# Optimization experiments

Hardware: AMD Instinct MI355X
Metric: run time of the kernel (lower is better)

The kernel has to match this reference:

```python
import jax, jax.numpy as jnp
import numpy as np

LN_EPS = 1e-5
ROPE_BASE = 10000.0


def rotate_half(x):
    # x: [..., d]; split into two halves (matches einops '(j d)->j d', j=2)
    d2 = x.shape[-1] // 2
    x1, x2 = x[..., :d2], x[..., d2:]
    return jnp.concatenate((-x2, x1), axis=-1)


def rotary_pos_emb(n, head_dim, dtype=jnp.float32):
    inv_freq = 1.0 / (ROPE_BASE ** (jnp.arange(0, head_dim, 2, dtype=jnp.float32) / head_dim))
    t = jnp.arange(n, dtype=jnp.float32)
    freqs = jnp.einsum('i,j->ij', t, inv_freq)          # [n, d/2]
    return jnp.concatenate((freqs, freqs), axis=-1).astype(dtype)  # [n, d]


def apply_rotary(pos, t):
    return t * jnp.cos(pos) + rotate_half(t) * jnp.sin(pos)


def setup_inputs() -> dict:
    key = jax.random.key(0)
    ks = jax.random.split(key, 4)
    b, n, dm = 2, 4096, 2048
    x = jax.random.normal(ks[0], (b, n, dm), dtype=jnp.float32)
    wq = jax.random.normal(ks[1], (dm, dm), dtype=jnp.float32) * (dm ** -0.5)
    wk = jax.random.normal(ks[2], (dm, dm), dtype=jnp.float32) * (dm ** -0.5)
    wv = jax.random.normal(ks[3], (dm, dm), dtype=jnp.float32) * (dm ** -0.5)
    return {
        'x': x,
        'ln_gamma': jnp.ones((dm,), jnp.float32),
        'ln_beta': jnp.zeros((dm,), jnp.float32),
        'wq': wq, 'wk': wk, 'wv': wv,
        'num_heads': 16,
    }


def reference(x, ln_gamma, ln_beta, wq, wk, wv, num_heads):
    b, n, dm = x.shape
    hd = dm // num_heads
    # LayerNorm (eps=1e-5, torch default)
    mu = jnp.mean(x, axis=-1, keepdims=True)
    var = jnp.mean(jnp.square(x - mu), axis=-1, keepdims=True)
    xn = (x - mu) * jax.lax.rsqrt(var + LN_EPS) * ln_gamma + ln_beta
    # QKV projections (nn.Linear, bias=False => x @ W.T; weights stored as [out,in])
    q = jnp.einsum('bnd,ed->bne', xn, wq)
    k = jnp.einsum('bnd,ed->bne', xn, wk)
    v = jnp.einsum('bnd,ed->bne', xn, wv)
    # b n (h d) -> b h n d
    split = lambda t: t.reshape(b, n, num_heads, hd).transpose(0, 2, 1, 3)
    q, k, v = split(q), split(k), split(v)
    pos = rotary_pos_emb(n, hd, x.dtype)  # [n, hd], broadcasts over b,h
    q = apply_rotary(pos, q)
    k = apply_rotary(pos, k)
    return q, k, v
```

## Files before the change

kernel.cpp:

```cpp
#include <hip/hip_runtime.h>
#include <hip/hip_bf16.h>


typedef float f32x4 __attribute__((ext_vector_type(4)));
typedef __bf16 bf16x8 __attribute__((ext_vector_type(8)));
typedef __bf16 bf16x4 __attribute__((ext_vector_type(4)));

#define DM    2048
#define NSEQ  4096
#define NH    16
#define HD    128
#define NROWS 8192
#define MAT_ELEMS (2ull*NH*NSEQ*HD)

typedef __attribute__((address_space(1))) const void GV;
typedef __attribute__((address_space(3))) void LV;
__device__ __forceinline__ void gload_lds16(const void* g, void* l) {
    __builtin_amdgcn_global_load_lds((GV*)g, (LV*)l, 16, 0, 0);
}

__global__ __launch_bounds__(256)
void lncvt_kernel(const float* __restrict__ x, const float* __restrict__ g,
                  const float* __restrict__ be,
                  const float* __restrict__ wq, const float* __restrict__ wk,
                  const float* __restrict__ wv,
                  __bf16* __restrict__ xnb, __bf16* __restrict__ wb) {
    int bid = blockIdx.x;
    int tid = threadIdx.x;
    if (bid < NROWS) {
        int row = bid;
        const float4* xr = (const float4*)(x + (size_t)row * DM);
        float4 v0 = xr[tid];
        float4 v1 = xr[tid + 256];
        float s  = v0.x + v0.y + v0.z + v0.w + v1.x + v1.y + v1.z + v1.w;
        float ss = v0.x*v0.x + v0.y*v0.y + v0.z*v0.z + v0.w*v0.w
                 + v1.x*v1.x + v1.y*v1.y + v1.z*v1.z + v1.w*v1.w;
#pragma unroll
        for (int o = 32; o > 0; o >>= 1) {
            s  += __shfl_down(s, o);
            ss += __shfl_down(ss, o);
        }
        __shared__ float red[10];
        int wave = tid >> 6, lane = tid & 63;
        if (lane == 0) { red[wave] = s; red[4 + wave] = ss; }
        __syncthreads();
        if (tid == 0) {
            float S  = red[0] + red[1] + red[2] + red[3];
            float SS = red[4] + red[5] + red[6] + red[7];
            float mu  = S * (1.0f / DM);
            float var = SS * (1.0f / DM) - mu * mu;
            red[8] = mu;
            red[9] = rsqrtf(var + 1e-5f);
        }
        __syncthreads();
        float mu = red[8], rs = red[9];

        const float4* gp = (const float4*)g;
        const float4* bp = (const float4*)be;
        bf16x4* orow = (bf16x4*)(xnb + (size_t)row * DM);
        {
            float4 g0 = gp[tid], b0 = bp[tid];
            bf16x4 o;
            o[0] = (__bf16)((v0.x - mu) * rs * g0.x + b0.x);
            o[1] = (__bf16)((v0.y - mu) * rs * g0.y + b0.y);
            o[2] = (__bf16)((v0.z - mu) * rs * g0.z + b0.z);
            o[3] = (__bf16)((v0.w - mu) * rs * g0.w + b0.w);
            orow[tid] = o;
        }
        {
            float4 g1 = gp[tid + 256], b1 = bp[tid + 256];
            bf16x4 o;
            o[0] = (__bf16)((v1.x - mu) * rs * g1.x + b1.x);
            o[1] = (__bf16)((v1.y - mu) * rs * g1.y + b1.y);
            o[2] = (__bf16)((v1.z - mu) * rs * g1.z + b1.z);
            o[3] = (__bf16)((v1.w - mu) * rs * g1.w + b1.w);
            orow[tid + 256] = o;
        }
    } else {
        int cb = bid - NROWS;
        const float* a = (cb < 2048) ? wq : (cb < 4096) ? wk : wv;
        size_t base = ((size_t)(cb & 2047) * 256 + tid) * 8;
        float4 v0 = *(const float4*)(a + base);
        float4 v1 = *(const float4*)(a + base + 4);
        bf16x8 r;
        r[0] = (__bf16)v0.x; r[1] = (__bf16)v0.y; r[2] = (__bf16)v0.z; r[3] = (__bf16)v0.w;
        r[4] = (__bf16)v1.x; r[5] = (__bf16)v1.y; r[6] = (__bf16)v1.z; r[7] = (__bf16)v1.w;
        *(bf16x8*)(wb + (size_t)(cb >> 11) * 4194304 + base) = r;
    }
}


__device__ __forceinline__ void loadA4(bf16x8 (&a)[4][2], const __bf16* Sp,
                                       int base, int mb, int o0) {
#pragma unroll
    for (int mi = 0; mi < 4; mi++)
#pragma unroll
        for (int ks = 0; ks < 2; ks++)
            a[mi][ks] = *(const bf16x8*)(Sp + base + (mb + mi) * 1024 + (o0 ^ (ks * 32)));
}
__device__ __forceinline__ void loadB2(bf16x8 (&b)[2][2], const __bf16* Sp,
                                       int base, int cb, int o0) {
#pragma unroll
    for (int f = 0; f < 2; f++)
#pragma unroll
        for (int ks = 0; ks < 2; ks++)
            b[f][ks] = *(const bf16x8*)(Sp + base + (f * 16 + (cb >> 1) * 64) * 64 + (o0 ^ (ks * 32)));
}

template<int RB, int CB>
__device__ __forceinline__ void cluster(f32x4 (&acc)[8][4], bf16x8 (&a)[4][2],
                                        bf16x8 (&b)[2][2]) {
    __builtin_amdgcn_s_setprio(1);
#pragma unroll
    for (int mi = 0; mi < 4; mi++)
#pragma unroll
        for (int ni = 0; ni < 2; ni++)
#pragma unroll
            for (int ks = 0; ks < 2; ks++)
                acc[RB + mi][CB + ni] = __builtin_amdgcn_mfma_f32_16x16x32_bf16(
                    a[mi][ks], b[ni][ks], acc[RB + mi][CB + ni], 0, 0, 0);
    __builtin_amdgcn_s_setprio(0);
}

#define FENCE asm volatile("" ::: "memory")
#define BAR   do { FENCE; __builtin_amdgcn_s_barrier(); FENCE; } while (0)
#define VM8   asm volatile("s_waitcnt vmcnt(8)" ::: "memory")
#define VM0   asm volatile("s_waitcnt vmcnt(0)" ::: "memory")

#define STGA(P, kt, HF) do { \
    gload_lds16(pA + (size_t)((HF) * 64 + w * 8) * DM + (kt) * 64,       &As[P][((HF) * 8 + w) * 512]); \
    gload_lds16(pA + (size_t)((HF) * 64 + 128 + w * 8) * DM + (kt) * 64, &As[P][((HF) * 8 + 16 + w) * 512]); \
} while (0)
#define STGB(P, kt, HF) do { \
    gload_lds16(pB + (size_t)((HF) * 64 + w * 8) * DM + (kt) * 64,       &Bs[P][((HF) * 8 + w) * 512]); \
    gload_lds16(pB + (size_t)((HF) * 64 + 128 + w * 8) * DM + (kt) * 64, &Bs[P][((HF) * 8 + 16 + w) * 512]); \
} while (0)

#define KTILE(kt, P, SG, W) do { \
    W; BAR; \
    loadA4(a,  &As[P][0], baseA, 0, o0); \
    loadB2(b0, &Bs[P][0], baseB, 0, o0); \
    loadB2(b1, &Bs[P][0], baseB, 2, o0); \
    cluster<0, 0>(acc, a, b0); \
    cluster<0, 2>(acc, a, b1); \
    loadA4(a, &As[P][0], baseA, 4, o0); \
    cluster<4, 0>(acc, a, b0); \
    cluster<4, 2>(acc, a, b1); \
    BAR; \
    if (SG) { STGA(P, (kt) + 2, 0); STGA(P, (kt) + 2, 1); \
              STGB(P, (kt) + 2, 0); STGB(P, (kt) + 2, 1); } \
} while (0)

__global__ __launch_bounds__(512, 2)
void gemm_qkv(const __bf16* __restrict__ A,
              const __bf16* __restrict__ Wq,
              const __bf16* __restrict__ Wk,
              const __bf16* __restrict__ Wv,
              float* __restrict__ out) {
    __shared__ __bf16 As[2][16384];
    __shared__ __bf16 Bs[2][16384];

    int tid = threadIdx.x;
    int w = tid >> 6, l = tid & 63;
    int wm = w >> 2, wn = w & 3;

    int bid = blockIdx.x;
    int x = bid & 7;
    int ridx = bid >> 3;
    int q = ridx >> 5;
    int s = ridx & 31;
    int mtp, ntp;
    if (q == 0)      { mtp = s >> 3;       ntp = s & 7; }
    else if (q == 1) { mtp = 4 + (s >> 3); ntp = s & 7; }
    else             { mtp = s & 7;        ntp = 8 + (s >> 3); }
    int mt = (x & 3) * 8 + mtp;
    int nt = (x >> 2) * 12 + ntp;
    int mat = nt >> 3, ntb = nt & 7;
    const __bf16* Wp = (mat == 0) ? Wq : (mat == 1) ? Wk : Wv;
    int row0 = mt * 256, colp = ntb * 256;

    int lr = l >> 3;
    int lco = ((l & 7) ^ lr) * 8;
    const __bf16* pA = A  + (size_t)(row0 + lr) * DM + lco;
    const __bf16* pB = Wp + (size_t)(colp + lr) * DM + lco;

    int baseA = (wm * 128 + (l & 15)) * 64;
    int baseB = ((wn & 1) * 32 + (wn >> 1) * 128 + (l & 15)) * 64;
    int o0 = ((l >> 4) * 8) ^ ((l & 7) * 8);

    STGA(0, 0, 0); STGA(0, 0, 1); STGB(0, 0, 0); STGB(0, 0, 1);
    STGA(1, 1, 0); STGA(1, 1, 1); STGB(1, 1, 0); STGB(1, 1, 1);

    f32x4 acc[8][4];
#pragma unroll
    for (int i = 0; i < 8; i++)
#pragma unroll
        for (int j = 0; j < 4; j++)
            acc[i][j] = (f32x4){0.f, 0.f, 0.f, 0.f};

    bf16x8 a[4][2], b0[2][2], b1[2][2];

#pragma unroll 1
    for (int kt = 0; kt < 30; kt += 2) {
        KTILE(kt,     0, 1, VM8);
        KTILE(kt + 1, 1, 1, VM8);
    }
    KTILE(30, 0, 0, VM8);
    KTILE(31, 1, 0, VM0);

    float* op = out + (size_t)mat * MAT_ELEMS;
    int hd_lo = (wn & 1) * 32 + (l & 15);
    int head = ntb * 2 + (wn >> 1);
    int r_base = row0 + wm * 128 + ((l >> 4) << 2);
    float if0 = exp2f(-0.20762051f * (float)hd_lo);
    float if1 = exp2f(-0.20762051f * (float)(hd_lo + 16));

    if (mat < 2) {
#pragma unroll
        for (int mi = 0; mi < 8; mi++) {
#pragma unroll
            for (int j = 0; j < 4; j++) {
                int r = r_base + mi * 16 + j;
                int b = r >> 12, n = r & 4095;
                float fn = (float)n;
                float* rowp = op + ((size_t)((b * NH + head) * NSEQ + n)) * HD;
#pragma unroll
                for (int ni = 0; ni < 2; ni++) {
                    float lo = acc[mi][ni][j], hi = acc[mi][ni + 2][j];
                    float sv, cv;
                    __sincosf(fn * (ni ? if1 : if0), &sv, &cv);
                    rowp[hd_lo + ni * 16]      = lo * cv - hi * sv;
                    rowp[hd_lo + ni * 16 + 64] = hi * cv + lo * sv;
                }
            }
        }
    } else {
#pragma unroll
        for (int mi = 0; mi < 8; mi++) {
#pragma unroll
            for (int j = 0; j < 4; j++) {
                int r = r_base + mi * 16 + j;
                int b = r >> 12, n = r & 4095;
                float* rowp = op + ((size_t)((b * NH + head) * NSEQ + n)) * HD;
#pragma unroll
                for (int ni = 0; ni < 2; ni++) {
                    rowp[hd_lo + ni * 16]      = acc[mi][ni][j];
                    rowp[hd_lo + ni * 16 + 64] = acc[mi][ni + 2][j];
                }
            }
        }
    }
}

extern "C" void kernel_launch(void* const* d_in, const int* in_sizes, int n_in,
                              void* d_out, int out_size, void* d_ws, size_t ws_size,
                              hipStream_t stream) {
    const float* x  = (const float*)d_in[0];
    const float* g  = (const float*)d_in[1];
    const float* be = (const float*)d_in[2];
    const float* wq = (const float*)d_in[3];
    const float* wk = (const float*)d_in[4];
    const float* wv = (const float*)d_in[5];
    float* out = (float*)d_out;

    char* ws = (char*)d_ws;
    __bf16* xnb = (__bf16*)ws;
    __bf16* wb  = (__bf16*)(ws + 33554432);

    lncvt_kernel<<<NROWS + 6144, 256, 0, stream>>>(x, g, be, wq, wk, wv, xnb, wb);
    gemm_qkv<<<768, 512, 0, stream>>>(xnb, wb, wb + 4194304, wb + 8388608, out);
}
```

Measured before the change: 228.3 us.

## Software-pipeline LDS fragment loads across k-tiles with register double buffering

Restructures the GEMM main loop so the next k-tile's A-low and B fragments are read from LDS into a second register set while the current tile's second half of MFMAs runs. The two barriers per k-tile become one, with explicit lgkmcnt/vmcnt waits and sched_barrier fences to pin the ordering. The aim is to hide LDS read latency behind MFMA work and cut synchronization. In exchange it adds extra fragment registers under a tight launch-bounds budget, which risks spilling. It also waits for all outstanding global loads each tile, which may reduce overlap of global prefetch.

```diff
diff --git a/kernel.cpp b/kernel.cpp
--- a/kernel.cpp
+++ b/kernel.cpp
@@ -122,10 +122,12 @@
     __builtin_amdgcn_s_setprio(0);
 }
 
-#define FENCE asm volatile("" ::: "memory")
-#define BAR   do { FENCE; __builtin_amdgcn_s_barrier(); FENCE; } while (0)
-#define VM8   asm volatile("s_waitcnt vmcnt(8)" ::: "memory")
-#define VM0   asm volatile("s_waitcnt vmcnt(0)" ::: "memory")
+#define FENCE  asm volatile("" ::: "memory")
+#define BAR    do { FENCE; __builtin_amdgcn_s_barrier(); FENCE; } while (0)
+#define LGKM0  asm volatile("s_waitcnt lgkmcnt(0)" ::: "memory")
+#define VM8    asm volatile("s_waitcnt vmcnt(8)" ::: "memory")
+#define VM0    asm volatile("s_waitcnt vmcnt(0)" ::: "memory")
+#define SCHED0 __builtin_amdgcn_sched_barrier(0)
 
 #define STGA(P, kt, HF) do { \
     gload_lds16(pA + (size_t)((HF) * 64 + w * 8) * DM + (kt) * 64,       &As[P][((HF) * 8 + w) * 512]); \
@@ -136,19 +138,21 @@
     gload_lds16(pB + (size_t)((HF) * 64 + 128 + w * 8) * DM + (kt) * 64, &Bs[P][((HF) * 8 + 16 + w) * 512]); \
 } while (0)
 
-#define KTILE(kt, P, SG, W) do { \
-    W; BAR; \
-    loadA4(a,  &As[P][0], baseA, 0, o0); \
-    loadB2(b0, &Bs[P][0], baseB, 0, o0); \
-    loadB2(b1, &Bs[P][0], baseB, 2, o0); \
-    cluster<0, 0>(acc, a, b0); \
-    cluster<0, 2>(acc, a, b1); \
-    loadA4(a, &As[P][0], baseA, 4, o0); \
-    cluster<4, 0>(acc, a, b0); \
-    cluster<4, 2>(acc, a, b1); \
-    BAR; \
+#define KTILE(kt, P, Q, SG, NX, BC0, BC1, BN0, BN1) do { \
+    loadA4(a_hi, &As[P][0], baseA, 4, o0);        \
+    SCHED0; \
+    cluster<0, 0>(acc, a_lo, BC0); \
+    cluster<0, 2>(acc, a_lo, BC1); \
+    SCHED0; \
+    LGKM0; VM0; BAR; \
     if (SG) { STGA(P, (kt) + 2, 0); STGA(P, (kt) + 2, 1); \
               STGB(P, (kt) + 2, 0); STGB(P, (kt) + 2, 1); } \
+    if (NX) { loadA4(a_lo, &As[Q][0], baseA, 0, o0); \
+              loadB2(BN0, &Bs[Q][0], baseB, 0, o0); \
+              loadB2(BN1, &Bs[Q][0], baseB, 2, o0); } \
+    SCHED0; \
+    cluster<4, 0>(acc, a_hi, BC0); \
+    cluster<4, 2>(acc, a_hi, BC1); \
 } while (0)
 
 __global__ __launch_bounds__(512, 2)
@@ -198,15 +202,24 @@
         for (int j = 0; j < 4; j++)
             acc[i][j] = (f32x4){0.f, 0.f, 0.f, 0.f};
 
-    bf16x8 a[4][2], b0[2][2], b1[2][2];
+    bf16x8 a_lo[4][2], a_hi[4][2];
+    bf16x8 bE0[2][2], bE1[2][2], bO0[2][2], bO1[2][2];
+
+    VM8;
+    BAR;
+    loadA4(a_lo, &As[0][0], baseA, 0, o0);
+    loadB2(bE0, &Bs[0][0], baseB, 0, o0);
+    loadB2(bE1, &Bs[0][0], baseB, 2, o0);
 
 #pragma unroll 1
-    for (int kt = 0; kt < 30; kt += 2) {
-        KTILE(kt,     0, 1, VM8);
-        KTILE(kt + 1, 1, 1, VM8);
+    for (int kt = 0; kt < 28; kt += 2) {
+        KTILE(kt,     0, 1, 1, 1, bE0, bE1, bO0, bO1);
+        KTILE(kt + 1, 1, 0, 1, 1, bO0, bO1, bE0, bE1);
     }
-    KTILE(30, 0, 0, VM8);
-    KTILE(31, 1, 0, VM0);
+    KTILE(28, 0, 1, 1, 1, bE0, bE1, bO0, bO1);
+    KTILE(29, 1, 0, 1, 1, bO0, bO1, bE0, bE1);
+    KTILE(30, 0, 1, 0, 1, bE0, bE1, bO0, bO1);
+    KTILE(31, 1, 0, 0, 0, bO0, bO1, bE0, bE1);
 
     float* op = out + (size_t)mat * MAT_ELEMS;
     int hd_lo = (wn & 1) * 32 + (l & 15);
```

Result: slower. 761.8 us (+233.7%).
